# Kernel tuning notes

Hardware: AMD Instinct MI355X
Metric: run time of the kernel (lower is better)

Reference implementation:

```python
import jax, jax.numpy as jnp
import numpy as np

B, H, W = 16, 128, 128
NUM_SAMPLES, HID = 16, 256


def setup_inputs() -> dict:
    key = jax.random.key(0)
    ks = jax.random.split(key, 12)
    inp = {
        "x": jax.random.uniform(ks[0], (B, H, W, 2), jnp.float32) * 2.0 - 1.0,
        "sample_idx": jax.random.randint(ks[1], (B,), 0, NUM_SAMPLES),
        "shift_vectors": jax.random.normal(ks[2], (NUM_SAMPLES, 2), jnp.float32) * 0.05,
        "rotation_angle": jax.random.normal(ks[3], (NUM_SAMPLES, 1), jnp.float32) * 0.05,
        "color_scales": 1.0 + jax.random.normal(ks[4], (NUM_SAMPLES, 3), jnp.float32) * 0.05,
        "color_shifts": jax.random.normal(ks[5], (NUM_SAMPLES, 3), jnp.float32) * 0.05,
        "W1": jax.random.normal(ks[6], (2, HID), jnp.float32) / np.sqrt(2.0),
        "b1": jnp.zeros((HID,), jnp.float32),
        "W2": jax.random.normal(ks[7], (HID, HID), jnp.float32) / np.sqrt(HID),
        "b2": jnp.zeros((HID,), jnp.float32),
        "W3": jax.random.normal(ks[8], (HID, HID), jnp.float32) / np.sqrt(HID),
        "b3": jnp.zeros((HID,), jnp.float32),
        "W4": jax.random.normal(ks[9], (HID, 3), jnp.float32) / np.sqrt(HID),
        "b4": jnp.zeros((3,), jnp.float32),
    }
    return inp


def reference(x, sample_idx, shift_vectors, rotation_angle, color_scales, color_shifts,
              W1, b1, W2, b2, W3, b3, W4, b4):
    # Per-sample affine coordinate transform (vectorized gather + batched 2x3 affine).
    shift = shift_vectors[sample_idx]            # [B,2] -> (dy, dx)
    dy, dx = shift[:, 0], shift[:, 1]
    ang = rotation_angle[sample_idx, 0]          # [B]
    c, s = jnp.cos(ang), jnp.sin(ang)
    rot = jnp.stack([jnp.stack([c, -s], -1),
                     jnp.stack([s, c], -1)], -2)  # [B,2,2]
    trans = jnp.stack([dx, dy], -1)               # [B,2]
    coords = jnp.einsum('bij,bhwj->bhwi', rot, x) + trans[:, None, None, :]

    # INR decoder MLP: coords -> RGB
    h = jax.nn.relu(coords @ W1 + b1)
    h = jax.nn.relu(h @ W2 + b2)
    h = jax.nn.relu(h @ W3 + b3)
    out = h @ W4 + b4                             # [B,H,W,3]

    # Per-sample color affine, skipped for reference sample idx==0.
    scales = color_scales[sample_idx][:, None, None, :]
    shifts = color_shifts[sample_idx][:, None, None, :]
    mask = (sample_idx != 0)[:, None, None, None]
    out = jnp.where(mask, out * scales + shifts, out)
    return out, dx, dy
```

## Files before the change

kernel.cpp:

```cpp
#include <hip/hip_runtime.h>
#include <math.h>

typedef _Float16 half8  __attribute__((ext_vector_type(8)));
typedef _Float16 half4v __attribute__((ext_vector_type(4)));
typedef float    f32x4  __attribute__((ext_vector_type(4)));

#define W1OFF 0
#define W2OFF 8192
#define W3OFF 73728
#define W4OFF 139264
#define SWTOT 143360
#define OUT_PIX (16*128*128)

__global__ void inr_prep(const float* __restrict__ W1, const float* __restrict__ W2,
                         const float* __restrict__ W3, const float* __restrict__ W4,
                         const int* __restrict__ sidx, const float* __restrict__ sv,
                         _Float16* __restrict__ wsw, float* __restrict__ outtail)
{
    int tid = blockIdx.x * 256 + threadIdx.x;
    if (tid < 16) {
        int si = sidx[tid];
        outtail[tid]      = sv[2*si + 1];
        outtail[16 + tid] = sv[2*si + 0];
    }
    if (tid >= SWTOT) return;
    int kind, rel;
    if      (tid < W2OFF) { kind = 0; rel = tid; }
    else if (tid < W3OFF) { kind = 1; rel = tid - W2OFF; }
    else if (tid < W4OFF) { kind = 2; rel = tid - W3OFF; }
    else                  { kind = 3; rel = tid - W4OFF; }
    int j    = rel & 7;
    int lane = (rel >> 3) & 63;
    int blk  = rel >> 9;
    int q = lane >> 4, ln = lane & 15;
    float val;
    if (kind == 3) {
        int m = ln;
        int k = blk * 32 + q * 8 + j;
        val = (m < 3) ? W4[k*3 + m] : 0.0f;
    } else {
        int MT = blk & 15, kkb = blk >> 4;
        int m = MT*16 + ln;
        int k = kkb*32 + q*8 + j;
        if      (kind == 0) val = (k < 2) ? W1[k*256 + m] : 0.0f;
        else if (kind == 1) val = W2[k*256 + m];
        else                val = W3[k*256 + m];
    }
    wsw[tid] = (_Float16)val;
}

template<int NKK>
__device__ __forceinline__ void do_layer(const half8* __restrict__ Asw,
                                         const float* __restrict__ bias,
                                         _Float16* hbuf, int wm, int wn,
                                         int q, int ln, int lane)
{
    f32x4 acc[4][4];
#pragma unroll
    for (int mt = 0; mt < 4; ++mt)
#pragma unroll
        for (int nt = 0; nt < 4; ++nt)
            acc[mt][nt] = (f32x4){0.f, 0.f, 0.f, 0.f};

#pragma unroll
    for (int kkb = 0; kkb < NKK; ++kkb) {
        half8 aw[4];
#pragma unroll
        for (int mt = 0; mt < 4; ++mt)
            aw[mt] = Asw[(kkb*16 + 4*wm + mt)*64 + lane];
        half8 bf[4];
        int g = kkb*4 + q;
#pragma unroll
        for (int nt = 0; nt < 4; ++nt)
            bf[nt] = *(const half8*)&hbuf[g*1024 + (wn*64 + 16*nt + ln)*8];
#pragma unroll
        for (int nt = 0; nt < 4; ++nt)
#pragma unroll
            for (int mt = 0; mt < 4; ++mt)
                acc[mt][nt] = __builtin_amdgcn_mfma_f32_16x16x32_f16(aw[mt], bf[nt], acc[mt][nt], 0, 0, 0);
    }
    __syncthreads();
#pragma unroll
    for (int mt = 0; mt < 4; ++mt) {
        int hid0 = 64*wm + 16*mt + 4*q;
        f32x4 bv = *(const f32x4*)&bias[hid0];
        int g = hid0 >> 3;
        int o = hid0 & 7;
#pragma unroll
        for (int nt = 0; nt < 4; ++nt) {
            int pixel = wn*64 + 16*nt + ln;
            f32x4 a = acc[mt][nt];
            half4v hv;
            hv[0] = (_Float16)fmaxf(a[0] + bv[0], 0.f);
            hv[1] = (_Float16)fmaxf(a[1] + bv[1], 0.f);
            hv[2] = (_Float16)fmaxf(a[2] + bv[2], 0.f);
            hv[3] = (_Float16)fmaxf(a[3] + bv[3], 0.f);
            *(half4v*)&hbuf[g*1024 + pixel*8 + o] = hv;
        }
    }
    __syncthreads();
}

__launch_bounds__(512, 4)
__global__ void inr_fused(const float* __restrict__ x, const int* __restrict__ sidx_p,
                          const float* __restrict__ sv, const float* __restrict__ ra,
                          const float* __restrict__ cs, const float* __restrict__ csh,
                          const float* __restrict__ b1, const float* __restrict__ b2,
                          const float* __restrict__ b3, const float* __restrict__ b4,
                          const _Float16* __restrict__ wsw, float* __restrict__ out)
{
    __shared__ __align__(16) _Float16 hbuf[32768];
    int t = threadIdx.x;
    int lane = t & 63, w = t >> 6, q = lane >> 4, ln = lane & 15;
    int wm = w & 3, wn = w >> 2;
    int pixbase = blockIdx.x * 128;
    int b = pixbase >> 14;
    int sidx = sidx_p[b];
    float dy = sv[2*sidx], dx = sv[2*sidx + 1];
    float ang = ra[sidx];
    float sn, cn;
    sincosf(ang, &sn, &cn);

    if (t < 128) {
        int p = t;
        float x0 = x[(pixbase + p)*2 + 0];
        float x1 = x[(pixbase + p)*2 + 1];
        float u = cn*x0 - sn*x1 + dx;
        float v = sn*x0 + cn*x1 + dy;
        half8 z;
#pragma unroll
        for (int i = 0; i < 8; ++i) z[i] = (_Float16)0.0f;
#pragma unroll
        for (int g = 1; g < 4; ++g)
            *(half8*)&hbuf[g*1024 + p*8] = z;
        z[0] = (_Float16)u; z[1] = (_Float16)v;
        *(half8*)&hbuf[0*1024 + p*8] = z;
    }
    __syncthreads();

    const half8* wsw8 = (const half8*)wsw;
    do_layer<1>(wsw8,                b1, hbuf, wm, wn, q, ln, lane);
    do_layer<8>(wsw8 + (W2OFF >> 3), b2, hbuf, wm, wn, q, ln, lane);
    do_layer<8>(wsw8 + (W3OFF >> 3), b3, hbuf, wm, wn, q, ln, lane);

    const half8* w4p = wsw8 + (W4OFF >> 3);
    f32x4 a4 = (f32x4){0.f,0.f,0.f,0.f};
#pragma unroll
    for (int kkb = 0; kkb < 8; ++kkb) {
        half8 aw = w4p[kkb*64 + lane];
        half8 bf = *(const half8*)&hbuf[(kkb*4 + q)*1024 + (16*w + ln)*8];
        a4 = __builtin_amdgcn_mfma_f32_16x16x32_f16(aw, bf, a4, 0, 0, 0);
    }
    if (q == 0) {
        bool doc = (sidx != 0);
        float s0 = cs[sidx*3+0], s1 = cs[sidx*3+1], s2 = cs[sidx*3+2];
        float t0 = csh[sidx*3+0], t1 = csh[sidx*3+1], t2 = csh[sidx*3+2];
        float v0 = a4[0] + b4[0];
        float v1 = a4[1] + b4[1];
        float v2 = a4[2] + b4[2];
        if (doc) { v0 = v0*s0 + t0; v1 = v1*s1 + t1; v2 = v2*s2 + t2; }
        int gp = pixbase + 16*w + ln;
        out[gp*3 + 0] = v0;
        out[gp*3 + 1] = v1;
        out[gp*3 + 2] = v2;
    }
}

extern "C" void kernel_launch(void* const* d_in, const int* in_sizes, int n_in,
                              void* d_out, int out_size, void* d_ws, size_t ws_size,
                              hipStream_t stream)
{
    const float* x    = (const float*)d_in[0];
    const int*   sidx = (const int*)  d_in[1];
    const float* sv   = (const float*)d_in[2];
    const float* ra   = (const float*)d_in[3];
    const float* cs   = (const float*)d_in[4];
    const float* csh  = (const float*)d_in[5];
    const float* W1   = (const float*)d_in[6];
    const float* b1   = (const float*)d_in[7];
    const float* W2   = (const float*)d_in[8];
    const float* b2   = (const float*)d_in[9];
    const float* W3   = (const float*)d_in[10];
    const float* b3   = (const float*)d_in[11];
    const float* W4   = (const float*)d_in[12];
    const float* b4   = (const float*)d_in[13];
    float* out = (float*)d_out;
    _Float16* wsw = (_Float16*)d_ws;

    inr_prep<<<SWTOT/256, 256, 0, stream>>>(W1, W2, W3, W4, sidx, sv, wsw, out + OUT_PIX*3);
    inr_fused<<<OUT_PIX/128, 512, 0, stream>>>(x, sidx, sv, ra, cs, csh,
                                               b1, b2, b3, b4, wsw, out);
}
```

Measured before the change: 150.0 us.

## Switch MLP layers to 32x32x16 MFMA with 4-wave blocks

Replaces the 16x16x32 MFMA tiles with 32x32x16 MFMA, re-swizzling the fp16 weights in the prep kernel to match the new operand layout. Each block now runs 4 waves instead of 8, each owning 64 hidden rows across all 128 pixels, and the first layer pads K only to 16. The larger MFMA tile is meant to raise operand reuse per instruction and cut LDS fragment reads. In exchange, there are fewer waves per block, more accumulator registers per wave, and the layer-4 output path changes.

```diff
diff --git a/kernel.cpp b/kernel.cpp
--- a/kernel.cpp
+++ b/kernel.cpp
@@ -3,12 +3,14 @@
 
 typedef _Float16 half8  __attribute__((ext_vector_type(8)));
 typedef _Float16 half4v __attribute__((ext_vector_type(4)));
+typedef __fp16   fp16x2 __attribute__((ext_vector_type(2)));
 typedef float    f32x4  __attribute__((ext_vector_type(4)));
+typedef float    f32x16 __attribute__((ext_vector_type(16)));
 
 #define W1OFF 0
-#define W2OFF 8192
-#define W3OFF 73728
-#define W4OFF 139264
+#define W2OFF 4096
+#define W3OFF 69632
+#define W4OFF 135168
 #define SWTOT 143360
 #define OUT_PIX (16*128*128)
 
@@ -32,76 +34,83 @@
     int j    = rel & 7;
     int lane = (rel >> 3) & 63;
     int blk  = rel >> 9;
-    int q = lane >> 4, ln = lane & 15;
+    int m32  = lane & 31;
+    int hsel = lane >> 5;
     float val;
     if (kind == 3) {
-        int m = ln;
-        int k = blk * 32 + q * 8 + j;
-        val = (m < 3) ? W4[k*3 + m] : 0.0f;
+        int k = blk*16 + hsel*8 + j;
+        val = (m32 < 3) ? W4[k*3 + m32] : 0.0f;
+    } else if (kind == 0) {
+        int m = blk*32 + m32;
+        int k = hsel*8 + j;
+        val = (k < 2) ? W1[k*256 + m] : 0.0f;
     } else {
-        int MT = blk & 15, kkb = blk >> 4;
-        int m = MT*16 + ln;
-        int k = kkb*32 + q*8 + j;
-        if      (kind == 0) val = (k < 2) ? W1[k*256 + m] : 0.0f;
-        else if (kind == 1) val = W2[k*256 + m];
-        else                val = W3[k*256 + m];
+        int MT = blk & 7, s = blk >> 3;
+        int m = MT*32 + m32;
+        int k = s*16 + hsel*8 + j;
+        val = (kind == 1) ? W2[k*256 + m] : W3[k*256 + m];
     }
     wsw[tid] = (_Float16)val;
 }
 
-template<int NKK>
+template<int NKS>
 __device__ __forceinline__ void do_layer(const half8* __restrict__ Asw,
                                          const float* __restrict__ bias,
-                                         _Float16* hbuf, int wm, int wn,
-                                         int q, int ln, int lane)
-{
-    f32x4 acc[4][4];
-#pragma unroll
-    for (int mt = 0; mt < 4; ++mt)
+                                         _Float16* hbuf, int w, int m32, int hsel, int lane)
+{
+    f32x16 acc[2][4];
+#pragma unroll
+    for (int mt = 0; mt < 2; ++mt)
 #pragma unroll
         for (int nt = 0; nt < 4; ++nt)
-            acc[mt][nt] = (f32x4){0.f, 0.f, 0.f, 0.f};
-
-#pragma unroll
-    for (int kkb = 0; kkb < NKK; ++kkb) {
-        half8 aw[4];
-#pragma unroll
-        for (int mt = 0; mt < 4; ++mt)
-            aw[mt] = Asw[(kkb*16 + 4*wm + mt)*64 + lane];
+#pragma unroll
+            for (int i = 0; i < 16; ++i)
+                acc[mt][nt][i] = 0.0f;
+
+#pragma unroll
+    for (int s = 0; s < NKS; ++s) {
+        half8 aw[2];
+#pragma unroll
+        for (int mt = 0; mt < 2; ++mt)
+            aw[mt] = Asw[(s*8 + 2*w + mt)*64 + lane];
         half8 bf[4];
-        int g = kkb*4 + q;
+        int g = s*2 + hsel;
 #pragma unroll
         for (int nt = 0; nt < 4; ++nt)
-            bf[nt] = *(const half8*)&hbuf[g*1024 + (wn*64 + 16*nt + ln)*8];
+            bf[nt] = *(const half8*)&hbuf[g*1024 + (32*nt + m32)*8];
 #pragma unroll
         for (int nt = 0; nt < 4; ++nt)
 #pragma unroll
-            for (int mt = 0; mt < 4; ++mt)
-                acc[mt][nt] = __builtin_amdgcn_mfma_f32_16x16x32_f16(aw[mt], bf[nt], acc[mt][nt], 0, 0, 0);
+            for (int mt = 0; mt < 2; ++mt)
+                acc[mt][nt] = __builtin_amdgcn_mfma_f32_32x32x16_f16(aw[mt], bf[nt], acc[mt][nt], 0, 0, 0);
     }
     __syncthreads();
 #pragma unroll
-    for (int mt = 0; mt < 4; ++mt) {
-        int hid0 = 64*wm + 16*mt + 4*q;
-        f32x4 bv = *(const f32x4*)&bias[hid0];
-        int g = hid0 >> 3;
-        int o = hid0 & 7;
-#pragma unroll
-        for (int nt = 0; nt < 4; ++nt) {
-            int pixel = wn*64 + 16*nt + ln;
-            f32x4 a = acc[mt][nt];
-            half4v hv;
-            hv[0] = (_Float16)fmaxf(a[0] + bv[0], 0.f);
-            hv[1] = (_Float16)fmaxf(a[1] + bv[1], 0.f);
-            hv[2] = (_Float16)fmaxf(a[2] + bv[2], 0.f);
-            hv[3] = (_Float16)fmaxf(a[3] + bv[3], 0.f);
-            *(half4v*)&hbuf[g*1024 + pixel*8 + o] = hv;
+    for (int mt = 0; mt < 2; ++mt) {
+#pragma unroll
+        for (int g4 = 0; g4 < 4; ++g4) {
+            int hid0 = 32*(2*w + mt) + 8*g4 + 4*hsel;
+            f32x4 bv = *(const f32x4*)&bias[hid0];
+            int gg = 4*(2*w + mt) + g4;
+            int o  = 4*hsel;
+#pragma unroll
+            for (int nt = 0; nt < 4; ++nt) {
+                int pixel = 32*nt + m32;
+                fp16x2 lo = __builtin_amdgcn_cvt_pkrtz(fmaxf(acc[mt][nt][4*g4+0] + bv[0], 0.f),
+                                                       fmaxf(acc[mt][nt][4*g4+1] + bv[1], 0.f));
+                fp16x2 hi = __builtin_amdgcn_cvt_pkrtz(fmaxf(acc[mt][nt][4*g4+2] + bv[2], 0.f),
+                                                       fmaxf(acc[mt][nt][4*g4+3] + bv[3], 0.f));
+                half4v hv;
+                hv[0] = (_Float16)lo[0]; hv[1] = (_Float16)lo[1];
+                hv[2] = (_Float16)hi[0]; hv[3] = (_Float16)hi[1];
+                *(half4v*)&hbuf[gg*1024 + pixel*8 + o] = hv;
+            }
         }
     }
     __syncthreads();
 }
 
-__launch_bounds__(512, 4)
+__launch_bounds__(256, 2)
 __global__ void inr_fused(const float* __restrict__ x, const int* __restrict__ sidx_p,
                           const float* __restrict__ sv, const float* __restrict__ ra,
                           const float* __restrict__ cs, const float* __restrict__ csh,
@@ -111,8 +120,8 @@
 {
     __shared__ __align__(16) _Float16 hbuf[32768];
     int t = threadIdx.x;
-    int lane = t & 63, w = t >> 6, q = lane >> 4, ln = lane & 15;
-    int wm = w & 3, wn = w >> 2;
+    int lane = t & 63, w = t >> 6;
+    int m32 = lane & 31, hsel = lane >> 5;
     int pixbase = blockIdx.x * 128;
     int b = pixbase >> 14;
     int sidx = sidx_p[b];
@@ -130,28 +139,28 @@
         half8 z;
 #pragma unroll
         for (int i = 0; i < 8; ++i) z[i] = (_Float16)0.0f;
-#pragma unroll
-        for (int g = 1; g < 4; ++g)
-            *(half8*)&hbuf[g*1024 + p*8] = z;
+        *(half8*)&hbuf[1*1024 + p*8] = z;
         z[0] = (_Float16)u; z[1] = (_Float16)v;
         *(half8*)&hbuf[0*1024 + p*8] = z;
     }
     __syncthreads();
 
     const half8* wsw8 = (const half8*)wsw;
-    do_layer<1>(wsw8,                b1, hbuf, wm, wn, q, ln, lane);
-    do_layer<8>(wsw8 + (W2OFF >> 3), b2, hbuf, wm, wn, q, ln, lane);
-    do_layer<8>(wsw8 + (W3OFF >> 3), b3, hbuf, wm, wn, q, ln, lane);
+    do_layer<1> (wsw8 + (W1OFF >> 3), b1, hbuf, w, m32, hsel, lane);
+    do_layer<16>(wsw8 + (W2OFF >> 3), b2, hbuf, w, m32, hsel, lane);
+    do_layer<16>(wsw8 + (W3OFF >> 3), b3, hbuf, w, m32, hsel, lane);
 
     const half8* w4p = wsw8 + (W4OFF >> 3);
-    f32x4 a4 = (f32x4){0.f,0.f,0.f,0.f};
-#pragma unroll
-    for (int kkb = 0; kkb < 8; ++kkb) {
-        half8 aw = w4p[kkb*64 + lane];
-        half8 bf = *(const half8*)&hbuf[(kkb*4 + q)*1024 + (16*w + ln)*8];
-        a4 = __builtin_amdgcn_mfma_f32_16x16x32_f16(aw, bf, a4, 0, 0, 0);
-    }
-    if (q == 0) {
+    f32x16 a4;
+#pragma unroll
+    for (int i = 0; i < 16; ++i) a4[i] = 0.0f;
+#pragma unroll
+    for (int s = 0; s < 16; ++s) {
+        half8 aw = w4p[s*64 + lane];
+        half8 bf = *(const half8*)&hbuf[(s*2 + hsel)*1024 + (32*w + m32)*8];
+        a4 = __builtin_amdgcn_mfma_f32_32x32x16_f16(aw, bf, a4, 0, 0, 0);
+    }
+    if (lane < 32) {
         bool doc = (sidx != 0);
         float s0 = cs[sidx*3+0], s1 = cs[sidx*3+1], s2 = cs[sidx*3+2];
         float t0 = csh[sidx*3+0], t1 = csh[sidx*3+1], t2 = csh[sidx*3+2];
@@ -159,7 +168,7 @@
         float v1 = a4[1] + b4[1];
         float v2 = a4[2] + b4[2];
         if (doc) { v0 = v0*s0 + t0; v1 = v1*s1 + t1; v2 = v2*s2 + t2; }
-        int gp = pixbase + 16*w + ln;
+        int gp = pixbase + 32*w + lane;
         out[gp*3 + 0] = v0;
         out[gp*3 + 1] = v1;
         out[gp*3 + 2] = v2;
@@ -188,6 +197,6 @@
     _Float16* wsw = (_Float16*)d_ws;
 
     inr_prep<<<SWTOT/256, 256, 0, stream>>>(W1, W2, W3, W4, sidx, sv, wsw, out + OUT_PIX*3);
-    inr_fused<<<OUT_PIX/128, 512, 0, stream>>>(x, sidx, sv, ra, cs, csh,
+    inr_fused<<<OUT_PIX/128, 256, 0, stream>>>(x, sidx, sv, ra, cs, csh,
                                                b1, b2, b3, b4, wsw, out);
 }
```

Measured after the change: 155.2 us. 1.03x slower.
